# Optimization experiments

Hardware: AMD Instinct MI355X
Metric: run time of the kernel (lower is better)

## Reference

```python
import jax, jax.numpy as jnp
import numpy as np

# ---- config (matches init_kwargs) ----
B, N, D = 16, 300, 256
HEADS, HD = 8, D // 8
FF = 1024
HID = FF // 2                      # SwiGLU hidden
SPATIAL = [(80, 80), (40, 40), (20, 20), (10, 10)]
LVL = len(SPATIAL)
NP = 4                              # points per level
TP = LVL * NP                       # total sampling points = 16
L = sum(h * w for h, w in SPATIAL)  # 8400
EPS = 1e-6


def setup_inputs() -> dict:
    key = jax.random.key(0)
    ks = jax.random.split(key, 24)
    s = 0.02
    return {
        "target": jax.random.normal(ks[0], (B, N, D), jnp.float32),
        "reference_points": jax.random.uniform(ks[1], (B, N, 1, 4), jnp.float32, 0.05, 0.95),
        "memory": jax.random.normal(ks[2], (B, L, D), jnp.float32),
        # self-attention
        "qkv_w": jax.random.normal(ks[3], (3 * D, D), jnp.float32) * s,
        "qkv_b": jnp.zeros((3 * D,), jnp.float32),
        "out_w": jax.random.normal(ks[4], (D, D), jnp.float32) * s,
        "out_b": jnp.zeros((D,), jnp.float32),
        "norm1_w": jnp.ones((D,), jnp.float32),
        # deformable cross-attention
        "off_w": jax.random.normal(ks[5], (HEADS * TP * 2, D), jnp.float32) * s,
        "off_b": jax.random.normal(ks[6], (HEADS * TP * 2,), jnp.float32) * 0.1,
        "aw_w": jax.random.normal(ks[7], (HEADS * TP, D), jnp.float32) * s,
        "aw_b": jnp.zeros((HEADS * TP,), jnp.float32),
        "cout_w": jax.random.normal(ks[8], (D, D), jnp.float32) * s,
        "cout_b": jnp.zeros((D,), jnp.float32),
        "norm2_w": jnp.ones((D,), jnp.float32),
        # SwiGLU FFN
        "w13": jax.random.normal(ks[9], (2 * HID, D), jnp.float32) * s,
        "w13_b": jnp.zeros((2 * HID,), jnp.float32),
        "w2": jax.random.normal(ks[10], (D, HID), jnp.float32) * s,
        "w2_b": jnp.zeros((D,), jnp.float32),
        "norm3_w": jnp.ones((D,), jnp.float32),
    }


def rmsnorm(x, w):
    return x * jax.lax.rsqrt(jnp.mean(x * x, axis=-1, keepdims=True) + EPS) * w


def bilinear_sample(vflat, loc, H, W):
    """vflat: (BH, hd, H*W); loc: (BH, Q, 2) in [0,1]. grid_sample align_corners=False, zero pad."""
    x = loc[..., 0] * W - 0.5
    y = loc[..., 1] * H - 0.5
    x0 = jnp.floor(x); y0 = jnp.floor(y)
    dx = x - x0; dy = y - y0
    x0i = x0.astype(jnp.int32); y0i = y0.astype(jnp.int32)

    def gather(xi, yi, w):
        valid = (xi >= 0) & (xi < W) & (yi >= 0) & (yi < H)
        idx = jnp.clip(yi, 0, H - 1) * W + jnp.clip(xi, 0, W - 1)
        g = jnp.take_along_axis(vflat, idx[:, None, :], axis=2)  # (BH, hd, Q)
        return g * (w * valid)[:, None, :]

    return (gather(x0i, y0i, (1 - dx) * (1 - dy))
            + gather(x0i + 1, y0i, dx * (1 - dy))
            + gather(x0i, y0i + 1, (1 - dx) * dy)
            + gather(x0i + 1, y0i + 1, dx * dy))


def reference(target, reference_points, memory, qkv_w, qkv_b, out_w, out_b, norm1_w,
              off_w, off_b, aw_w, aw_b, cout_w, cout_b, norm2_w,
              w13, w13_b, w2, w2_b, norm3_w):
    # ---------- self-attention (query_pos_embed=None, attn_mask=None) ----------
    qkv = target @ qkv_w.T + qkv_b                    # (B,N,3D)
    qkv = qkv.reshape(B, N, 3, HEADS, HD).transpose(2, 0, 3, 1, 4)
    q, k, v = qkv[0], qkv[1], qkv[2]                  # (B,H,N,hd)
    attn = jax.nn.softmax(jnp.einsum("bhqd,bhkd->bhqk", q, k) / np.sqrt(HD), axis=-1)
    sa = jnp.einsum("bhqk,bhkd->bhqd", attn, v).transpose(0, 2, 1, 3).reshape(B, N, D)
    x = rmsnorm(target + (sa @ out_w.T + out_b), norm1_w)

    # ---------- deformable cross-attention ----------
    # value_op: memory -> per-head value (B,H,hd,L)
    val = memory.reshape(B, L, HEADS, HD).transpose(0, 2, 3, 1).reshape(B * HEADS, HD, L)

    offsets = (x @ off_w.T + off_b).reshape(B, N, HEADS, TP, 2)
    aw = jax.nn.softmax((x @ aw_w.T + aw_b).reshape(B, N, HEADS, TP), axis=-1)

    ref_xy = reference_points[:, :, :, None, :2]      # (B,N,1,1,2)
    ref_wh = reference_points[:, :, :, None, 2:]
    pts_scale = 1.0 / NP
    loc = ref_xy + offsets * pts_scale * ref_wh * 0.5  # (B,N,H,TP,2)
    loc = loc.transpose(0, 2, 1, 3, 4).reshape(B * HEADS, N, TP, 2)

    sampled = []
    start = 0
    for li, (H, W) in enumerate(SPATIAL):
        v_l = jax.lax.dynamic_slice_in_dim(val, start, H * W, axis=2)
        loc_l = loc[:, :, li * NP:(li + 1) * NP, :].reshape(B * HEADS, N * NP, 2)
        s = bilinear_sample(v_l, loc_l, H, W).reshape(B * HEADS, HD, N, NP)
        sampled.append(s)
        start += H * W
    sampled = jnp.concatenate(sampled, axis=-1)        # (BH, hd, N, TP)

    w = aw.transpose(0, 2, 1, 3).reshape(B * HEADS, 1, N, TP)
    ca = (sampled * w).sum(-1)                         # (BH, hd, N)
    ca = ca.reshape(B, HEADS, HD, N).transpose(0, 3, 1, 2).reshape(B, N, D)
    ca = ca @ cout_w.T + cout_b

    x = rmsnorm(x + ca, norm2_w)

    # ---------- SwiGLU FFN ----------
    h = x @ w13.T + w13_b
    h1, h2 = h[..., :HID], h[..., HID:]
    ffn = (jax.nn.silu(h1) * h2) @ w2.T + w2_b
    x = jnp.clip(x + ffn, -65504.0, 65504.0)
    return rmsnorm(x, norm3_w)
```

## Files before the change

kernel.cpp:

```cpp
#include <hip/hip_runtime.h>
#include <cstdint>
#include <cstddef>


typedef __attribute__((ext_vector_type(8))) short bf16x8;
typedef __attribute__((ext_vector_type(4))) float f32x4;

__device__ __forceinline__ unsigned short f2bf(float f) {
  unsigned int u = __float_as_uint(f);
  u = (u + 0x7fffu + ((u >> 16) & 1u)) >> 16;
  return (unsigned short)u;
}
__device__ __forceinline__ unsigned int pack2bf(float lo, float hi) {
  return ((unsigned int)f2bf(hi) << 16) | (unsigned int)f2bf(lo);
}

__device__ __forceinline__ void gemm_dev(
    const float* __restrict__ A, const float* __restrict__ W,
    const float* __restrict__ bias, float* __restrict__ C,
    int N, int K, int row0, int col0,
    unsigned short* As, unsigned short* Ws)
{
  const int t = threadIdx.x, wave = t >> 6, lane = t & 63;
  const int lr = lane & 15, g = lane >> 4;
  const int sr = t >> 4, sc = (t & 15) * 4;

  float4 ra[4], rw[8];
  const float* Ab = A + (size_t)(row0 + sr) * K + sc;
  const float* Wb = W + (size_t)(col0 + sr) * K + sc;

#pragma unroll
  for (int i = 0; i < 4; ++i) ra[i] = *(const float4*)(Ab + (size_t)16 * i * K);
#pragma unroll
  for (int j = 0; j < 8; ++j) rw[j] = *(const float4*)(Wb + (size_t)16 * j * K);

  f32x4 acc[4][2] = {};

  for (int k0 = 0; k0 < K; k0 += 64) {
    __syncthreads();
#pragma unroll
    for (int i = 0; i < 4; ++i) {
      uint2 p;
      p.x = pack2bf(ra[i].x, ra[i].y);
      p.y = pack2bf(ra[i].z, ra[i].w);
      *(uint2*)&As[(sr + 16 * i) * 72 + sc] = p;
    }
#pragma unroll
    for (int j = 0; j < 8; ++j) {
      uint2 p;
      p.x = pack2bf(rw[j].x, rw[j].y);
      p.y = pack2bf(rw[j].z, rw[j].w);
      *(uint2*)&Ws[(sr + 16 * j) * 72 + sc] = p;
    }
    __syncthreads();

    if (k0 + 64 < K) {
#pragma unroll
      for (int i = 0; i < 4; ++i)
        ra[i] = *(const float4*)(Ab + (size_t)16 * i * K + k0 + 64);
#pragma unroll
      for (int j = 0; j < 8; ++j)
        rw[j] = *(const float4*)(Wb + (size_t)16 * j * K + k0 + 64);
    }

#pragma unroll
    for (int ks = 0; ks < 2; ++ks) {
      bf16x8 aA[4], bB[2];
#pragma unroll
      for (int i = 0; i < 4; ++i)
        aA[i] = *(const bf16x8*)&As[(i * 16 + lr) * 72 + ks * 32 + g * 8];
#pragma unroll
      for (int j = 0; j < 2; ++j)
        bB[j] = *(const bf16x8*)&Ws[(wave * 32 + j * 16 + lr) * 72 + ks * 32 + g * 8];
#pragma unroll
      for (int i = 0; i < 4; ++i)
#pragma unroll
        for (int j = 0; j < 2; ++j)
          acc[i][j] = __builtin_amdgcn_mfma_f32_16x16x32_bf16(aA[i], bB[j], acc[i][j], 0, 0, 0);
    }
  }

  const float b0 = bias[col0 + wave * 32 + lr];
  const float b1 = bias[col0 + wave * 32 + 16 + lr];
#pragma unroll
  for (int i = 0; i < 4; ++i) {
#pragma unroll
    for (int r = 0; r < 4; ++r) {
      const int row = row0 + i * 16 + g * 4 + r;
      float* dst = &C[(size_t)row * N + col0 + wave * 32 + lr];
      dst[0]  = acc[i][0][r] + b0;
      dst[16] = acc[i][1][r] + b1;
    }
  }
}

__global__ __launch_bounds__(256) void gemm_mfma(
    const float* __restrict__ A, const float* __restrict__ W,
    const float* __restrict__ bias, float* __restrict__ C, int N, int K)
{
  __shared__ __align__(16) unsigned short As[64 * 72];
  __shared__ __align__(16) unsigned short Ws[128 * 72];
  gemm_dev(A, W, bias, C, N, K, blockIdx.y * 64, blockIdx.x * 128, As, Ws);
}

__global__ __launch_bounds__(256) void gemm_offaw(
    const float* __restrict__ X,
    const float* __restrict__ off_w, const float* __restrict__ off_b, float* __restrict__ OF,
    const float* __restrict__ aw_w, const float* __restrict__ aw_b, float* __restrict__ AW,
    int K)
{
  __shared__ __align__(16) unsigned short As[64 * 72];
  __shared__ __align__(16) unsigned short Ws[128 * 72];
  if (blockIdx.x < 2)
    gemm_dev(X, off_w, off_b, OF, 256, K, blockIdx.y * 64, blockIdx.x * 128, As, Ws);
  else
    gemm_dev(X, aw_w, aw_b, AW, 128, K, blockIdx.y * 64, 0, As, Ws);
}

template <bool SWIGLU>
__global__ __launch_bounds__(256) void gemm_rms32(
    const float* __restrict__ A, const float* __restrict__ W,
    const float* __restrict__ bias, const float* __restrict__ res,
    const float* __restrict__ nw, float* __restrict__ C,
    int K, int clip)
{
  __shared__ __align__(16) unsigned short As[32 * 72];
  __shared__ __align__(16) unsigned short Ws[256 * 72];
  __shared__ float rsum[32][4];

  const int t = threadIdx.x, wave = t >> 6, lane = t & 63;
  const int lr = lane & 15, g = lane >> 4;
  const int row0 = blockIdx.x * 32;
  const int sr = t >> 4, sc = (t & 15) * 4;
  const int Astride = SWIGLU ? 1024 : K;

  float4 ra1[2], ra2[2], rw[16];
  const float* Ab = A + (size_t)(row0 + sr) * Astride + sc;
  const float* Wb = W + (size_t)sr * K + sc;

#pragma unroll
  for (int i = 0; i < 2; ++i) {
    ra1[i] = *(const float4*)(Ab + (size_t)16 * i * Astride);
    if (SWIGLU) ra2[i] = *(const float4*)(Ab + (size_t)16 * i * Astride + 512);
  }
#pragma unroll
  for (int j = 0; j < 16; ++j) rw[j] = *(const float4*)(Wb + (size_t)16 * j * K);

  f32x4 acc[2][4] = {};

  for (int k0 = 0; k0 < K; k0 += 64) {
    __syncthreads();
#pragma unroll
    for (int i = 0; i < 2; ++i) {
      float4 v;
      if (SWIGLU) {
        v.x = ra1[i].x / (1.f + __expf(-ra1[i].x)) * ra2[i].x;
        v.y = ra1[i].y / (1.f + __expf(-ra1[i].y)) * ra2[i].y;
        v.z = ra1[i].z / (1.f + __expf(-ra1[i].z)) * ra2[i].z;
        v.w = ra1[i].w / (1.f + __expf(-ra1[i].w)) * ra2[i].w;
      } else {
        v = ra1[i];
      }
      uint2 p;
      p.x = pack2bf(v.x, v.y);
      p.y = pack2bf(v.z, v.w);
      *(uint2*)&As[(sr + 16 * i) * 72 + sc] = p;
    }
#pragma unroll
    for (int j = 0; j < 16; ++j) {
      uint2 p;
      p.x = pack2bf(rw[j].x, rw[j].y);
      p.y = pack2bf(rw[j].z, rw[j].w);
      *(uint2*)&Ws[(sr + 16 * j) * 72 + sc] = p;
    }
    __syncthreads();

    if (k0 + 64 < K) {
#pragma unroll
      for (int i = 0; i < 2; ++i) {
        ra1[i] = *(const float4*)(Ab + (size_t)16 * i * Astride + k0 + 64);
        if (SWIGLU) ra2[i] = *(const float4*)(Ab + (size_t)16 * i * Astride + 512 + k0 + 64);
      }
#pragma unroll
      for (int j = 0; j < 16; ++j)
        rw[j] = *(const float4*)(Wb + (size_t)16 * j * K + k0 + 64);
    }

#pragma unroll
    for (int ks = 0; ks < 2; ++ks) {
      bf16x8 aA[2], bB[4];
#pragma unroll
      for (int i = 0; i < 2; ++i)
        aA[i] = *(const bf16x8*)&As[(i * 16 + lr) * 72 + ks * 32 + g * 8];
#pragma unroll
      for (int j = 0; j < 4; ++j)
        bB[j] = *(const bf16x8*)&Ws[(wave * 64 + j * 16 + lr) * 72 + ks * 32 + g * 8];
#pragma unroll
      for (int i = 0; i < 2; ++i)
#pragma unroll
        for (int j = 0; j < 4; ++j)
          acc[i][j] = __builtin_amdgcn_mfma_f32_16x16x32_bf16(aA[i], bB[j], acc[i][j], 0, 0, 0);
    }
  }

  float bj[4], wj[4];
#pragma unroll
  for (int j = 0; j < 4; ++j) {
    bj[j] = bias[wave * 64 + j * 16 + lr];
    wj[j] = nw[wave * 64 + j * 16 + lr];
  }

  float part[2][4] = {};
#pragma unroll
  for (int i = 0; i < 2; ++i) {
#pragma unroll
    for (int r = 0; r < 4; ++r) {
      const int row = row0 + i * 16 + g * 4 + r;
#pragma unroll
      for (int j = 0; j < 4; ++j) {
        const int col = wave * 64 + j * 16 + lr;
        float v = acc[i][j][r] + bj[j] + res[(size_t)row * 256 + col];
        if (clip) v = fminf(fmaxf(v, -65504.f), 65504.f);
        acc[i][j][r] = v;
        part[i][r] += v * v;
      }
    }
  }
#pragma unroll
  for (int i = 0; i < 2; ++i)
#pragma unroll
    for (int r = 0; r < 4; ++r) {
      float s = part[i][r];
      s += __shfl_xor(s, 1);
      s += __shfl_xor(s, 2);
      s += __shfl_xor(s, 4);
      s += __shfl_xor(s, 8);
      part[i][r] = s;
    }
  if (lr == 0) {
#pragma unroll
    for (int i = 0; i < 2; ++i)
#pragma unroll
      for (int r = 0; r < 4; ++r)
        rsum[i * 16 + g * 4 + r][wave] = part[i][r];
  }
  __syncthreads();

#pragma unroll
  for (int i = 0; i < 2; ++i) {
#pragma unroll
    for (int r = 0; r < 4; ++r) {
      const int row = row0 + i * 16 + g * 4 + r;
      const f32x4 q = *(const f32x4*)&rsum[i * 16 + g * 4 + r][0];
      const float tot = q[0] + q[1] + q[2] + q[3];
      const float scale = rsqrtf(tot * (1.0f / 256.0f) + 1e-6f);
#pragma unroll
      for (int j = 0; j < 4; ++j) {
        const int col = wave * 64 + j * 16 + lr;
        C[(size_t)row * 256 + col] = acc[i][j][r] * scale * wj[j];
      }
    }
  }
}

__global__ __launch_bounds__(256) void gemm_qkv(
    const float* __restrict__ A, const float* __restrict__ W,
    const float* __restrict__ bias,
    unsigned short* __restrict__ Qb, unsigned short* __restrict__ Kb,
    unsigned short* __restrict__ VTb)
{
  __shared__ __align__(16) unsigned short As[64 * 72];
  __shared__ __align__(16) unsigned short Ws[128 * 72];
  const int K = 256;
  const int t = threadIdx.x, wave = t >> 6, lane = t & 63;
  const int lr = lane & 15, g = lane >> 4;
  const int row0 = blockIdx.y * 64, col0 = blockIdx.x * 128;
  const int sr = t >> 4, sc = (t & 15) * 4;

  float4 ra[4], rw[8];
  const float* Ab = A + (size_t)(row0 + sr) * K + sc;
  const float* Wb = W + (size_t)(col0 + sr) * K + sc;

#pragma unroll
  for (int i = 0; i < 4; ++i) ra[i] = *(const float4*)(Ab + (size_t)16 * i * K);
#pragma unroll
  for (int j = 0; j < 8; ++j) rw[j] = *(const float4*)(Wb + (size_t)16 * j * K);

  f32x4 acc[4][2] = {};

  for (int k0 = 0; k0 < K; k0 += 64) {
    __syncthreads();
#pragma unroll
    for (int i = 0; i < 4; ++i) {
      uint2 p;
      p.x = pack2bf(ra[i].x, ra[i].y);
      p.y = pack2bf(ra[i].z, ra[i].w);
      *(uint2*)&As[(sr + 16 * i) * 72 + sc] = p;
    }
#pragma unroll
    for (int j = 0; j < 8; ++j) {
      uint2 p;
      p.x = pack2bf(rw[j].x, rw[j].y);
      p.y = pack2bf(rw[j].z, rw[j].w);
      *(uint2*)&Ws[(sr + 16 * j) * 72 + sc] = p;
    }
    __syncthreads();

    if (k0 + 64 < K) {
#pragma unroll
      for (int i = 0; i < 4; ++i)
        ra[i] = *(const float4*)(Ab + (size_t)16 * i * K + k0 + 64);
#pragma unroll
      for (int j = 0; j < 8; ++j)
        rw[j] = *(const float4*)(Wb + (size_t)16 * j * K + k0 + 64);
    }

#pragma unroll
    for (int ks = 0; ks < 2; ++ks) {
      bf16x8 aA[4], bB[2];
#pragma unroll
      for (int i = 0; i < 4; ++i)
        aA[i] = *(const bf16x8*)&As[(i * 16 + lr) * 72 + ks * 32 + g * 8];
#pragma unroll
      for (int j = 0; j < 2; ++j)
        bB[j] = *(const bf16x8*)&Ws[(wave * 32 + j * 16 + lr) * 72 + ks * 32 + g * 8];
#pragma unroll
      for (int i = 0; i < 4; ++i)
#pragma unroll
        for (int j = 0; j < 2; ++j)
          acc[i][j] = __builtin_amdgcn_mfma_f32_16x16x32_bf16(aA[i], bB[j], acc[i][j], 0, 0, 0);
    }
  }

  const int bx = blockIdx.x;
  const float scale = 0.17677669529663687f;
  const float b0 = bias[col0 + wave * 32 + lr];
  const float b1 = bias[col0 + wave * 32 + 16 + lr];

  if (bx < 4) {
    unsigned short* dstT = (bx < 2) ? Qb : Kb;
    const float mul = (bx < 2) ? scale : 1.0f;
#pragma unroll
    for (int i = 0; i < 4; ++i) {
#pragma unroll
      for (int r = 0; r < 4; ++r) {
        const int row = row0 + i * 16 + g * 4 + r;
        const int b = row / 300, n = row - b * 300;
#pragma unroll
        for (int j = 0; j < 2; ++j) {
          const int c768 = col0 + wave * 32 + j * 16 + lr;
          const int h = (c768 >> 5) & 7, c = c768 & 31;
          const float v = (acc[i][j][r] + (j ? b1 : b0)) * mul;
          dstT[((size_t)(b * 8 + h) * 304 + n) * 32 + c] = f2bf(v);
        }
      }
    }
  } else {
    __syncthreads();
#pragma unroll
    for (int i = 0; i < 4; ++i)
#pragma unroll
      for (int r = 0; r < 4; ++r)
#pragma unroll
        for (int j = 0; j < 2; ++j) {
          const int c_local = wave * 32 + j * 16 + lr;
          const int n_local = i * 16 + g * 4 + r;
          Ws[c_local * 72 + n_local] = f2bf(acc[i][j][r] + (j ? b1 : b0));
        }
    __syncthreads();
    for (int idx = t; idx < 128 * 64; idx += 256) {
      const int c_local = idx >> 6, n_local = idx & 63;
      const int row = row0 + n_local;
      const int b = row / 300, n = row - b * 300;
      const int c768 = col0 + c_local;
      const int h = (c768 >> 5) & 7, c = c768 & 31;
      VTb[((size_t)(b * 8 + h) * 32 + c) * 320 + n] = Ws[c_local * 72 + n_local];
    }
    if (blockIdx.y == 74) {
      for (int idx = t; idx < 64 * 32 * 20; idx += 256) {
        const int n = 300 + idx % 20;
        const int rem = idx / 20;
        const int c = rem & 31, bh4 = rem >> 5;
        const int b = bh4 >> 2, h = (bx - 4) * 4 + (bh4 & 3);
        VTb[((size_t)(b * 8 + h) * 32 + c) * 320 + n] = 0;
      }
    }
  }
}

__global__ __launch_bounds__(64) void attn_core(
    const unsigned short* __restrict__ Qb, const unsigned short* __restrict__ Kb,
    const unsigned short* __restrict__ VTb, float* __restrict__ sa)
{
  __shared__ __align__(16) unsigned short P[16 * 40];
  const int gt = blockIdx.x;
  const int bh = blockIdx.y, b = bh >> 3, h = bh & 7;
  const int lane = threadIdx.x, lr = lane & 15, g = lane >> 4;

  const unsigned short* Kbase = Kb + (size_t)bh * 304 * 32;
  const unsigned short* Vbase = VTb + (size_t)bh * 32 * 320;

  bf16x8 aQ = *(const bf16x8*)&Qb[((size_t)bh * 304 + gt * 16 + lr) * 32 + g * 8];

  f32x4 s[19];
  const f32x4 zero = {0.f, 0.f, 0.f, 0.f};
#pragma unroll
  for (int kt = 0; kt < 19; ++kt) {
    bf16x8 bK = *(const bf16x8*)&Kbase[(kt * 16 + lr) * 32 + g * 8];
    s[kt] = __builtin_amdgcn_mfma_f32_16x16x32_bf16(aQ, bK, zero, 0, 0, 0);
  }
  if (lr >= 12) {
    s[18][0] = -1e30f; s[18][1] = -1e30f; s[18][2] = -1e30f; s[18][3] = -1e30f;
  }

  float inv[4];
#pragma unroll
  for (int r = 0; r < 4; ++r) {
    float m = -1e30f;
#pragma unroll
    for (int kt = 0; kt < 19; ++kt) m = fmaxf(m, s[kt][r]);
#pragma unroll
    for (int o = 8; o >= 1; o >>= 1) m = fmaxf(m, __shfl_xor(m, o));
    float sum = 0.f;
#pragma unroll
    for (int kt = 0; kt < 19; ++kt) {
      float e = __expf(s[kt][r] - m);
      s[kt][r] = e;
      sum += e;
    }
#pragma unroll
    for (int o = 8; o >= 1; o >>= 1) sum += __shfl_xor(sum, o);
    inv[r] = 1.f / sum;
  }

  f32x4 o0 = {0.f, 0.f, 0.f, 0.f}, o1 = {0.f, 0.f, 0.f, 0.f};
#pragma unroll
  for (int ks = 0; ks < 10; ++ks) {
#pragma unroll
    for (int tp = 0; tp < 2; ++tp) {
      const int kt = ks * 2 + tp;
#pragma unroll
      for (int r = 0; r < 4; ++r) {
        unsigned short pv = (kt < 19) ? f2bf(s[kt][r]) : (unsigned short)0;
        P[(g * 4 + r) * 40 + tp * 16 + lr] = pv;
      }
    }
    asm volatile("s_waitcnt lgkmcnt(0)" ::: "memory");
    __builtin_amdgcn_sched_barrier(0);
    bf16x8 aP = *(const bf16x8*)&P[lr * 40 + g * 8];
    bf16x8 bV0 = *(const bf16x8*)&Vbase[(size_t)lr * 320 + ks * 32 + g * 8];
    bf16x8 bV1 = *(const bf16x8*)&Vbase[(size_t)(16 + lr) * 320 + ks * 32 + g * 8];
    o0 = __builtin_amdgcn_mfma_f32_16x16x32_bf16(aP, bV0, o0, 0, 0, 0);
    o1 = __builtin_amdgcn_mfma_f32_16x16x32_bf16(aP, bV1, o1, 0, 0, 0);
  }

#pragma unroll
  for (int r = 0; r < 4; ++r) {
    const int q = gt * 16 + g * 4 + r;
    if (q < 300) {
      const float iv = inv[r];
      float* dst = &sa[((size_t)b * 300 + q) * 256 + h * 32];
      dst[lr] = o0[r] * iv;
      dst[16 + lr] = o1[r] * iv;
    }
  }
}

__global__ __launch_bounds__(256) void deform_k(
    const float* __restrict__ memory, const float* __restrict__ refp,
    const float* __restrict__ OFF, const float* __restrict__ AW,
    float* __restrict__ ca)
{
  __shared__ float locx[8][16], locy[8][16], wgt[8][16];
  const int bn = blockIdx.x, b = bn / 300, t = threadIdx.x;

  if (t < 128) {
    int h = t >> 4, p = t & 15;
    float cx = refp[(size_t)bn * 4 + 0], cy = refp[(size_t)bn * 4 + 1];
    float rw = refp[(size_t)bn * 4 + 2], rh = refp[(size_t)bn * 4 + 3];
    float ox = OFF[(size_t)bn * 256 + h * 32 + p * 2 + 0];
    float oy = OFF[(size_t)bn * 256 + h * 32 + p * 2 + 1];
    locx[h][p] = cx + ox * 0.125f * rw;
    locy[h][p] = cy + oy * 0.125f * rh;
    float av = AW[(size_t)bn * 128 + t];
    float mx = av;
#pragma unroll
    for (int o = 8; o; o >>= 1) mx = fmaxf(mx, __shfl_xor(mx, o));
    float e = __expf(av - mx);
    float ssum = e;
#pragma unroll
    for (int o = 8; o; o >>= 1) ssum += __shfl_xor(ssum, o);
    wgt[h][p] = e / ssum;
  }
  __syncthreads();

  const int h = t >> 5, hd = t & 31;
  const float* mb = memory + (size_t)b * 8500 * 256 + h * 32 + hd;
  float acc = 0.f;
#pragma unroll
  for (int p = 0; p < 16; ++p) {
    const int HWs[4] = {80, 40, 20, 10};
    const int Sts[4] = {0, 6400, 8000, 8400};
    const int li = p >> 2;
    const int Hh = HWs[li], Ww = HWs[li], st = Sts[li];
    float x = locx[h][p] * (float)Ww - 0.5f;
    float y = locy[h][p] * (float)Hh - 0.5f;
    float x0f = floorf(x), y0f = floorf(y);
    float dx = x - x0f, dy = y - y0f;
    int x0 = (int)x0f, y0 = (int)y0f;
    float awp = wgt[h][p];
#pragma unroll
    for (int cc = 0; cc < 4; ++cc) {
      int xi = x0 + (cc & 1), yi = y0 + (cc >> 1);
      float wc = ((cc & 1) ? dx : 1.f - dx) * ((cc >> 1) ? dy : 1.f - dy);
      bool valid = (xi >= 0) && (xi < Ww) && (yi >= 0) && (yi < Hh);
      int xc = xi < 0 ? 0 : (xi >= Ww ? Ww - 1 : xi);
      int yc = yi < 0 ? 0 : (yi >= Hh ? Hh - 1 : yi);
      float gv = mb[(size_t)(st + yc * Ww + xc) * 256];
      acc += gv * (valid ? wc * awp : 0.f);
    }
  }
  ca[(size_t)bn * 256 + t] = acc;
}

extern "C" void kernel_launch(void* const* d_in, const int* in_sizes, int n_in,
                              void* d_out, int out_size, void* d_ws, size_t ws_size,
                              hipStream_t stream)
{
  (void)in_sizes; (void)n_in; (void)out_size; (void)ws_size;
  const float* target  = (const float*)d_in[0];
  const float* refp    = (const float*)d_in[1];
  const float* memory  = (const float*)d_in[2];
  const float* qkv_w   = (const float*)d_in[3];
  const float* qkv_b   = (const float*)d_in[4];
  const float* out_w   = (const float*)d_in[5];
  const float* out_b   = (const float*)d_in[6];
  const float* norm1_w = (const float*)d_in[7];
  const float* off_w   = (const float*)d_in[8];
  const float* off_b   = (const float*)d_in[9];
  const float* aw_w    = (const float*)d_in[10];
  const float* aw_b    = (const float*)d_in[11];
  const float* cout_w  = (const float*)d_in[12];
  const float* cout_b  = (const float*)d_in[13];
  const float* norm2_w = (const float*)d_in[14];
  const float* w13     = (const float*)d_in[15];
  const float* w13_b   = (const float*)d_in[16];
  const float* w2      = (const float*)d_in[17];
  const float* w2_b    = (const float*)d_in[18];
  const float* norm3_w = (const float*)d_in[19];
  float* out = (float*)d_out;

  float* ws  = (float*)d_ws;
  float* SA  = ws;
  float* X   = SA  + 4800 * 256;
  float* OF  = X   + 4800 * 256;
  float* AWb = OF  + 4800 * 256;
  float* CA  = AWb + 4800 * 128;
  float* X2  = CA  + 4800 * 256;
  float* Hb  = X2  + 4800 * 256;
  unsigned short* Qb  = (unsigned short*)(Hb + 4800 * 1024);
  unsigned short* Kb  = Qb + 128 * 304 * 32;
  unsigned short* VTb = Kb + 128 * 304 * 32;

  dim3 blk(256);

  gemm_qkv<<<dim3(6, 75), blk, 0, stream>>>(target, qkv_w, qkv_b, Qb, Kb, VTb);
  attn_core<<<dim3(19, 128), dim3(64), 0, stream>>>(Qb, Kb, VTb, SA);
  gemm_rms32<false><<<150, blk, 0, stream>>>(SA, out_w, out_b, target, norm1_w, X, 256, 0);
  gemm_offaw<<<dim3(3, 75), blk, 0, stream>>>(X, off_w, off_b, OF, aw_w, aw_b, AWb, 256);
  deform_k<<<4800, blk, 0, stream>>>(memory, refp, OF, AWb, CA);
  gemm_rms32<false><<<150, blk, 0, stream>>>(CA, cout_w, cout_b, X, norm2_w, X2, 256, 0);
  gemm_mfma<<<dim3(8, 75), blk, 0, stream>>>(X2, w13, w13_b, Hb, 1024, 256);
  gemm_rms32<true><<<150, blk, 0, stream>>>(Hb, w2, w2_b, X2, norm3_w, out, 512, 1);
}
```

Measured before the change: 131.0 us.

## Pre-convert weights and activations to bf16 so GEMMs load bf16 directly

Adds a conversion kernel that turns the target and all weight matrices into bf16 at the start of every call. Intermediate activations (self-attention output, deformable output, normed X and X2) are also written as bf16 mirrors. The GEMMs then load bf16 tiles with 16-byte loads and skip per-tile packing. This halves global read traffic and removes conversion ALU work inside the GEMM loops, at the cost of one extra launch and extra bf16 writes.

```diff
diff --git a/kernel.cpp b/kernel.cpp
--- a/kernel.cpp
+++ b/kernel.cpp
@@ -15,52 +15,83 @@
   return ((unsigned int)f2bf(hi) << 16) | (unsigned int)f2bf(lo);
 }
 
-__device__ __forceinline__ void gemm_dev(
-    const float* __restrict__ A, const float* __restrict__ W,
-    const float* __restrict__ bias, float* __restrict__ C,
-    int N, int K, int row0, int col0,
-    unsigned short* As, unsigned short* Ws)
+__global__ __launch_bounds__(256) void conv_w(
+    const float* __restrict__ s0, const float* __restrict__ s1,
+    const float* __restrict__ s2, const float* __restrict__ s3,
+    const float* __restrict__ s4, const float* __restrict__ s5,
+    const float* __restrict__ s6, const float* __restrict__ s7,
+    unsigned short* __restrict__ d0, unsigned short* __restrict__ d1,
+    unsigned short* __restrict__ d2, unsigned short* __restrict__ d3,
+    unsigned short* __restrict__ d4, unsigned short* __restrict__ d5,
+    unsigned short* __restrict__ d6, unsigned short* __restrict__ d7)
+{
+  const int sizes[8] = {1228800, 196608, 65536, 65536, 32768, 65536, 262144, 131072};
+  const float* s; unsigned short* d;
+  switch (blockIdx.y) {
+    case 0: s = s0; d = d0; break;
+    case 1: s = s1; d = d1; break;
+    case 2: s = s2; d = d2; break;
+    case 3: s = s3; d = d3; break;
+    case 4: s = s4; d = d4; break;
+    case 5: s = s5; d = d5; break;
+    case 6: s = s6; d = d6; break;
+    default: s = s7; d = d7; break;
+  }
+  const int n = sizes[blockIdx.y];
+  const int i4 = (blockIdx.x * 256 + threadIdx.x) * 4;
+  if (i4 >= n) return;
+  float4 v = *(const float4*)&s[i4];
+  uint2 p;
+  p.x = pack2bf(v.x, v.y);
+  p.y = pack2bf(v.z, v.w);
+  *(uint2*)&d[i4] = p;
+}
+
+__device__ __forceinline__ void gemm_core16(
+    const unsigned short* __restrict__ A16, const unsigned short* __restrict__ W16,
+    int K, int row0, int col0,
+    unsigned short* As, unsigned short* Ws, f32x4 acc[4][2])
 {
   const int t = threadIdx.x, wave = t >> 6, lane = t & 63;
   const int lr = lane & 15, g = lane >> 4;
-  const int sr = t >> 4, sc = (t & 15) * 4;
-
-  float4 ra[4], rw[8];
-  const float* Ab = A + (size_t)(row0 + sr) * K + sc;
-  const float* Wb = W + (size_t)(col0 + sr) * K + sc;
-
-#pragma unroll
-  for (int i = 0; i < 4; ++i) ra[i] = *(const float4*)(Ab + (size_t)16 * i * K);
-#pragma unroll
-  for (int j = 0; j < 8; ++j) rw[j] = *(const float4*)(Wb + (size_t)16 * j * K);
-
-  f32x4 acc[4][2] = {};
+
+  uint4 rA[2], rW[4];
+#pragma unroll
+  for (int i = 0; i < 2; ++i) {
+    const int c = t + i * 256, row = c >> 3, sl = c & 7;
+    rA[i] = *(const uint4*)&A16[(size_t)(row0 + row) * K + sl * 8];
+  }
+#pragma unroll
+  for (int j = 0; j < 4; ++j) {
+    const int c = t + j * 256, row = c >> 3, sl = c & 7;
+    rW[j] = *(const uint4*)&W16[(size_t)(col0 + row) * K + sl * 8];
+  }
 
   for (int k0 = 0; k0 < K; k0 += 64) {
     __syncthreads();
 #pragma unroll
-    for (int i = 0; i < 4; ++i) {
-      uint2 p;
-      p.x = pack2bf(ra[i].x, ra[i].y);
-      p.y = pack2bf(ra[i].z, ra[i].w);
-      *(uint2*)&As[(sr + 16 * i) * 72 + sc] = p;
-    }
-#pragma unroll
-    for (int j = 0; j < 8; ++j) {
-      uint2 p;
-      p.x = pack2bf(rw[j].x, rw[j].y);
-      p.y = pack2bf(rw[j].z, rw[j].w);
-      *(uint2*)&Ws[(sr + 16 * j) * 72 + sc] = p;
+    for (int i = 0; i < 2; ++i) {
+      const int c = t + i * 256, row = c >> 3, sl = c & 7;
+      *(uint4*)&As[row * 72 + sl * 8] = rA[i];
+    }
+#pragma unroll
+    for (int j = 0; j < 4; ++j) {
+      const int c = t + j * 256, row = c >> 3, sl = c & 7;
+      *(uint4*)&Ws[row * 72 + sl * 8] = rW[j];
     }
     __syncthreads();
 
     if (k0 + 64 < K) {
 #pragma unroll
-      for (int i = 0; i < 4; ++i)
-        ra[i] = *(const float4*)(Ab + (size_t)16 * i * K + k0 + 64);
-#pragma unroll
-      for (int j = 0; j < 8; ++j)
-        rw[j] = *(const float4*)(Wb + (size_t)16 * j * K + k0 + 64);
+      for (int i = 0; i < 2; ++i) {
+        const int c = t + i * 256, row = c >> 3, sl = c & 7;
+        rA[i] = *(const uint4*)&A16[(size_t)(row0 + row) * K + k0 + 64 + sl * 8];
+      }
+#pragma unroll
+      for (int j = 0; j < 4; ++j) {
+        const int c = t + j * 256, row = c >> 3, sl = c & 7;
+        rW[j] = *(const uint4*)&W16[(size_t)(col0 + row) * K + k0 + 64 + sl * 8];
+      }
     }
 
 #pragma unroll
@@ -79,7 +110,20 @@
           acc[i][j] = __builtin_amdgcn_mfma_f32_16x16x32_bf16(aA[i], bB[j], acc[i][j], 0, 0, 0);
     }
   }
-
+}
+
+__global__ __launch_bounds__(256) void gemm_mfma16(
+    const unsigned short* __restrict__ A16, const unsigned short* __restrict__ W16,
+    const float* __restrict__ bias, float* __restrict__ C, int N, int K)
+{
+  __shared__ __align__(16) unsigned short As[64 * 72];
+  __shared__ __align__(16) unsigned short Ws[128 * 72];
+  const int row0 = blockIdx.y * 64, col0 = blockIdx.x * 128;
+  f32x4 acc[4][2] = {};
+  gemm_core16(A16, W16, K, row0, col0, As, Ws, acc);
+
+  const int t = threadIdx.x, wave = t >> 6, lane = t & 63;
+  const int lr = lane & 15, g = lane >> 4;
   const float b0 = bias[col0 + wave * 32 + lr];
   const float b1 = bias[col0 + wave * 32 + 16 + lr];
 #pragma unroll
@@ -94,244 +138,56 @@
   }
 }
 
-__global__ __launch_bounds__(256) void gemm_mfma(
-    const float* __restrict__ A, const float* __restrict__ W,
-    const float* __restrict__ bias, float* __restrict__ C, int N, int K)
+__global__ __launch_bounds__(256) void gemm_offaw16(
+    const unsigned short* __restrict__ X16,
+    const unsigned short* __restrict__ off16, const float* __restrict__ off_b,
+    float* __restrict__ OF,
+    const unsigned short* __restrict__ aw16, const float* __restrict__ aw_b,
+    float* __restrict__ AW)
 {
   __shared__ __align__(16) unsigned short As[64 * 72];
   __shared__ __align__(16) unsigned short Ws[128 * 72];
-  gemm_dev(A, W, bias, C, N, K, blockIdx.y * 64, blockIdx.x * 128, As, Ws);
-}
-
-__global__ __launch_bounds__(256) void gemm_offaw(
-    const float* __restrict__ X,
-    const float* __restrict__ off_w, const float* __restrict__ off_b, float* __restrict__ OF,
-    const float* __restrict__ aw_w, const float* __restrict__ aw_b, float* __restrict__ AW,
-    int K)
-{
-  __shared__ __align__(16) unsigned short As[64 * 72];
-  __shared__ __align__(16) unsigned short Ws[128 * 72];
-  if (blockIdx.x < 2)
-    gemm_dev(X, off_w, off_b, OF, 256, K, blockIdx.y * 64, blockIdx.x * 128, As, Ws);
-  else
-    gemm_dev(X, aw_w, aw_b, AW, 128, K, blockIdx.y * 64, 0, As, Ws);
-}
-
-template <bool SWIGLU>
-__global__ __launch_bounds__(256) void gemm_rms32(
-    const float* __restrict__ A, const float* __restrict__ W,
-    const float* __restrict__ bias, const float* __restrict__ res,
-    const float* __restrict__ nw, float* __restrict__ C,
-    int K, int clip)
-{
-  __shared__ __align__(16) unsigned short As[32 * 72];
-  __shared__ __align__(16) unsigned short Ws[256 * 72];
-  __shared__ float rsum[32][4];
+  const int row0 = blockIdx.y * 64;
+  const bool isOff = blockIdx.x < 2;
+  const int col0 = isOff ? blockIdx.x * 128 : 0;
+  const unsigned short* W16 = isOff ? off16 : aw16;
+  const float* bias = isOff ? off_b : aw_b;
+  float* C = isOff ? OF : AW;
+  const int N = isOff ? 256 : 128;
+
+  f32x4 acc[4][2] = {};
+  gemm_core16(X16, W16, 256, row0, col0, As, Ws, acc);
 
   const int t = threadIdx.x, wave = t >> 6, lane = t & 63;
   const int lr = lane & 15, g = lane >> 4;
-  const int row0 = blockIdx.x * 32;
-  const int sr = t >> 4, sc = (t & 15) * 4;
-  const int Astride = SWIGLU ? 1024 : K;
-
-  float4 ra1[2], ra2[2], rw[16];
-  const float* Ab = A + (size_t)(row0 + sr) * Astride + sc;
-  const float* Wb = W + (size_t)sr * K + sc;
-
-#pragma unroll
-  for (int i = 0; i < 2; ++i) {
-    ra1[i] = *(const float4*)(Ab + (size_t)16 * i * Astride);
-    if (SWIGLU) ra2[i] = *(const float4*)(Ab + (size_t)16 * i * Astride + 512);
-  }
-#pragma unroll
-  for (int j = 0; j < 16; ++j) rw[j] = *(const float4*)(Wb + (size_t)16 * j * K);
-
-  f32x4 acc[2][4] = {};
-
-  for (int k0 = 0; k0 < K; k0 += 64) {
-    __syncthreads();
-#pragma unroll
-    for (int i = 0; i < 2; ++i) {
-      float4 v;
-      if (SWIGLU) {
-        v.x = ra1[i].x / (1.f + __expf(-ra1[i].x)) * ra2[i].x;
-        v.y = ra1[i].y / (1.f + __expf(-ra1[i].y)) * ra2[i].y;
-        v.z = ra1[i].z / (1.f + __expf(-ra1[i].z)) * ra2[i].z;
-        v.w = ra1[i].w / (1.f + __expf(-ra1[i].w)) * ra2[i].w;
-      } else {
-        v = ra1[i];
-      }
-      uint2 p;
-      p.x = pack2bf(v.x, v.y);
-      p.y = pack2bf(v.z, v.w);
-      *(uint2*)&As[(sr + 16 * i) * 72 + sc] = p;
-    }
-#pragma unroll
-    for (int j = 0; j < 16; ++j) {
-      uint2 p;
-      p.x = pack2bf(rw[j].x, rw[j].y);
-      p.y = pack2bf(rw[j].z, rw[j].w);
-      *(uint2*)&Ws[(sr + 16 * j) * 72 + sc] = p;
-    }
-    __syncthreads();
-
-    if (k0 + 64 < K) {
-#pragma unroll
-      for (int i = 0; i < 2; ++i) {
-        ra1[i] = *(const float4*)(Ab + (size_t)16 * i * Astride + k0 + 64);
-        if (SWIGLU) ra2[i] = *(const float4*)(Ab + (size_t)16 * i * Astride + 512 + k0 + 64);
-      }
-#pragma unroll
-      for (int j = 0; j < 16; ++j)
-        rw[j] = *(const float4*)(Wb + (size_t)16 * j * K + k0 + 64);
-    }
-
-#pragma unroll
-    for (int ks = 0; ks < 2; ++ks) {
-      bf16x8 aA[2], bB[4];
-#pragma unroll
-      for (int i = 0; i < 2; ++i)
-        aA[i] = *(const bf16x8*)&As[(i * 16 + lr) * 72 + ks * 32 + g * 8];
-#pragma unroll
-      for (int j = 0; j < 4; ++j)
-        bB[j] = *(const bf16x8*)&Ws[(wave * 64 + j * 16 + lr) * 72 + ks * 32 + g * 8];
-#pragma unroll
-      for (int i = 0; i < 2; ++i)
-#pragma unroll
-        for (int j = 0; j < 4; ++j)
-          acc[i][j] = __builtin_amdgcn_mfma_f32_16x16x32_bf16(aA[i], bB[j], acc[i][j], 0, 0, 0);
-    }
-  }
-
-  float bj[4], wj[4];
-#pragma unroll
-  for (int j = 0; j < 4; ++j) {
-    bj[j] = bias[wave * 64 + j * 16 + lr];
-    wj[j] = nw[wave * 64 + j * 16 + lr];
-  }
-
-  float part[2][4] = {};
-#pragma unroll
-  for (int i = 0; i < 2; ++i) {
+  const float b0 = bias[col0 + wave * 32 + lr];
+  const float b1 = bias[col0 + wave * 32 + 16 + lr];
+#pragma unroll
+  for (int i = 0; i < 4; ++i) {
 #pragma unroll
     for (int r = 0; r < 4; ++r) {
       const int row = row0 + i * 16 + g * 4 + r;
-#pragma unroll
-      for (int j = 0; j < 4; ++j) {
-        const int col = wave * 64 + j * 16 + lr;
-        float v = acc[i][j][r] + bj[j] + res[(size_t)row * 256 + col];
-        if (clip) v = fminf(fmaxf(v, -65504.f), 65504.f);
-        acc[i][j][r] = v;
-        part[i][r] += v * v;
-      }
-    }
-  }
-#pragma unroll
-  for (int i = 0; i < 2; ++i)
-#pragma unroll
-    for (int r = 0; r < 4; ++r) {
-      float s = part[i][r];
-      s += __shfl_xor(s, 1);
-      s += __shfl_xor(s, 2);
-      s += __shfl_xor(s, 4);
-      s += __shfl_xor(s, 8);
-      part[i][r] = s;
-    }
-  if (lr == 0) {
-#pragma unroll
-    for (int i = 0; i < 2; ++i)
-#pragma unroll
-      for (int r = 0; r < 4; ++r)
-        rsum[i * 16 + g * 4 + r][wave] = part[i][r];
-  }
-  __syncthreads();
-
-#pragma unroll
-  for (int i = 0; i < 2; ++i) {
-#pragma unroll
-    for (int r = 0; r < 4; ++r) {
-      const int row = row0 + i * 16 + g * 4 + r;
-      const f32x4 q = *(const f32x4*)&rsum[i * 16 + g * 4 + r][0];
-      const float tot = q[0] + q[1] + q[2] + q[3];
-      const float scale = rsqrtf(tot * (1.0f / 256.0f) + 1e-6f);
-#pragma unroll
-      for (int j = 0; j < 4; ++j) {
-        const int col = wave * 64 + j * 16 + lr;
-        C[(size_t)row * 256 + col] = acc[i][j][r] * scale * wj[j];
-      }
-    }
-  }
-}
-
-__global__ __launch_bounds__(256) void gemm_qkv(
-    const float* __restrict__ A, const float* __restrict__ W,
+      float* dst = &C[(size_t)row * N + col0 + wave * 32 + lr];
+      dst[0]  = acc[i][0][r] + b0;
+      dst[16] = acc[i][1][r] + b1;
+    }
+  }
+}
+
+__global__ __launch_bounds__(256) void gemm_qkv16(
+    const unsigned short* __restrict__ T16, const unsigned short* __restrict__ W16,
     const float* __restrict__ bias,
     unsigned short* __restrict__ Qb, unsigned short* __restrict__ Kb,
     unsigned short* __restrict__ VTb)
 {
   __shared__ __align__(16) unsigned short As[64 * 72];
   __shared__ __align__(16) unsigned short Ws[128 * 72];
-  const int K = 256;
+  const int row0 = blockIdx.y * 64, col0 = blockIdx.x * 128;
+  f32x4 acc[4][2] = {};
+  gemm_core16(T16, W16, 256, row0, col0, As, Ws, acc);
+
   const int t = threadIdx.x, wave = t >> 6, lane = t & 63;
   const int lr = lane & 15, g = lane >> 4;
-  const int row0 = blockIdx.y * 64, col0 = blockIdx.x * 128;
-  const int sr = t >> 4, sc = (t & 15) * 4;
-
-  float4 ra[4], rw[8];
-  const float* Ab = A + (size_t)(row0 + sr) * K + sc;
-  const float* Wb = W + (size_t)(col0 + sr) * K + sc;
-
-#pragma unroll
-  for (int i = 0; i < 4; ++i) ra[i] = *(const float4*)(Ab + (size_t)16 * i * K);
-#pragma unroll
-  for (int j = 0; j < 8; ++j) rw[j] = *(const float4*)(Wb + (size_t)16 * j * K);
-
-  f32x4 acc[4][2] = {};
-
-  for (int k0 = 0; k0 < K; k0 += 64) {
-    __syncthreads();
-#pragma unroll
-    for (int i = 0; i < 4; ++i) {
-      uint2 p;
-      p.x = pack2bf(ra[i].x, ra[i].y);
-      p.y = pack2bf(ra[i].z, ra[i].w);
-      *(uint2*)&As[(sr + 16 * i) * 72 + sc] = p;
-    }
-#pragma unroll
-    for (int j = 0; j < 8; ++j) {
-      uint2 p;
-      p.x = pack2bf(rw[j].x, rw[j].y);
-      p.y = pack2bf(rw[j].z, rw[j].w);
-      *(uint2*)&Ws[(sr + 16 * j) * 72 + sc] = p;
-    }
-    __syncthreads();
-
-    if (k0 + 64 < K) {
-#pragma unroll
-      for (int i = 0; i < 4; ++i)
-        ra[i] = *(const float4*)(Ab + (size_t)16 * i * K + k0 + 64);
-#pragma unroll
-      for (int j = 0; j < 8; ++j)
-        rw[j] = *(const float4*)(Wb + (size_t)16 * j * K + k0 + 64);
-    }
-
-#pragma unroll
-    for (int ks = 0; ks < 2; ++ks) {
-      bf16x8 aA[4], bB[2];
-#pragma unroll
-      for (int i = 0; i < 4; ++i)
-        aA[i] = *(const bf16x8*)&As[(i * 16 + lr) * 72 + ks * 32 + g * 8];
-#pragma unroll
-      for (int j = 0; j < 2; ++j)
-        bB[j] = *(const bf16x8*)&Ws[(wave * 32 + j * 16 + lr) * 72 + ks * 32 + g * 8];
-#pragma unroll
-      for (int i = 0; i < 4; ++i)
-#pragma unroll
-        for (int j = 0; j < 2; ++j)
-          acc[i][j] = __builtin_amdgcn_mfma_f32_16x16x32_bf16(aA[i], bB[j], acc[i][j], 0, 0, 0);
-    }
-  }
-
   const int bx = blockIdx.x;
   const float scale = 0.17677669529663687f;
   const float b0 = bias[col0 + wave * 32 + lr];
@@ -388,9 +244,172 @@
   }
 }
 
+template <bool SWIGLU>
+__global__ __launch_bounds__(256) void gemm_rms32_16(
+    const void* __restrict__ Ain, const unsigned short* __restrict__ W16,
+    const float* __restrict__ bias, const float* __restrict__ res,
+    const float* __restrict__ nw, float* __restrict__ C,
+    unsigned short* __restrict__ Cmir, int K, int clip)
+{
+  __shared__ __align__(16) unsigned short As[32 * 72];
+  __shared__ __align__(16) unsigned short Ws[256 * 72];
+  __shared__ float rsum[32][4];
+
+  const int t = threadIdx.x, wave = t >> 6, lane = t & 63;
+  const int lr = lane & 15, g = lane >> 4;
+  const int row0 = blockIdx.x * 32;
+  const int sr = t >> 4, sc = (t & 15) * 4;
+
+  uint4 rA;
+  float4 ra1[2], ra2[2];
+  uint4 rW[8];
+  const unsigned short* A16 = (const unsigned short*)Ain;
+  const float* Af = (const float*)Ain;
+
+  if (SWIGLU) {
+#pragma unroll
+    for (int i = 0; i < 2; ++i) {
+      ra1[i] = *(const float4*)&Af[(size_t)(row0 + sr + 16 * i) * 1024 + sc];
+      ra2[i] = *(const float4*)&Af[(size_t)(row0 + sr + 16 * i) * 1024 + 512 + sc];
+    }
+  } else {
+    const int row = t >> 3, sl = t & 7;
+    rA = *(const uint4*)&A16[(size_t)(row0 + row) * K + sl * 8];
+  }
+#pragma unroll
+  for (int j = 0; j < 8; ++j) {
+    const int c = t + j * 256, row = c >> 3, sl = c & 7;
+    rW[j] = *(const uint4*)&W16[(size_t)row * K + sl * 8];
+  }
+
+  f32x4 acc[2][4] = {};
+
+  for (int k0 = 0; k0 < K; k0 += 64) {
+    __syncthreads();
+    if (SWIGLU) {
+#pragma unroll
+      for (int i = 0; i < 2; ++i) {
+        float4 v;
+        v.x = ra1[i].x / (1.f + __expf(-ra1[i].x)) * ra2[i].x;
+        v.y = ra1[i].y / (1.f + __expf(-ra1[i].y)) * ra2[i].y;
+        v.z = ra1[i].z / (1.f + __expf(-ra1[i].z)) * ra2[i].z;
+        v.w = ra1[i].w / (1.f + __expf(-ra1[i].w)) * ra2[i].w;
+        uint2 p;
+        p.x = pack2bf(v.x, v.y);
+        p.y = pack2bf(v.z, v.w);
+        *(uint2*)&As[(sr + 16 * i) * 72 + sc] = p;
+      }
+    } else {
+      const int row = t >> 3, sl = t & 7;
+      *(uint4*)&As[row * 72 + sl * 8] = rA;
+    }
+#pragma unroll
+    for (int j = 0; j < 8; ++j) {
+      const int c = t + j * 256, row = c >> 3, sl = c & 7;
+      *(uint4*)&Ws[row * 72 + sl * 8] = rW[j];
+    }
+    __syncthreads();
+
+    if (k0 + 64 < K) {
+      if (SWIGLU) {
+#pragma unroll
+        for (int i = 0; i < 2; ++i) {
+          ra1[i] = *(const float4*)&Af[(size_t)(row0 + sr + 16 * i) * 1024 + k0 + 64 + sc];
+          ra2[i] = *(const float4*)&Af[(size_t)(row0 + sr + 16 * i) * 1024 + 512 + k0 + 64 + sc];
+        }
+      } else {
+        const int row = t >> 3, sl = t & 7;
+        rA = *(const uint4*)&A16[(size_t)(row0 + row) * K + k0 + 64 + sl * 8];
+      }
+#pragma unroll
+      for (int j = 0; j < 8; ++j) {
+        const int c = t + j * 256, row = c >> 3, sl = c & 7;
+        rW[j] = *(const uint4*)&W16[(size_t)row * K + k0 + 64 + sl * 8];
+      }
+    }
+
+#pragma unroll
+    for (int ks = 0; ks < 2; ++ks) {
+      bf16x8 aA[2], bB[4];
+#pragma unroll
+      for (int i = 0; i < 2; ++i)
+        aA[i] = *(const bf16x8*)&As[(i * 16 + lr) * 72 + ks * 32 + g * 8];
+#pragma unroll
+      for (int j = 0; j < 4; ++j)
+        bB[j] = *(const bf16x8*)&Ws[(wave * 64 + j * 16 + lr) * 72 + ks * 32 + g * 8];
+#pragma unroll
+      for (int i = 0; i < 2; ++i)
+#pragma unroll
+        for (int j = 0; j < 4; ++j)
+          acc[i][j] = __builtin_amdgcn_mfma_f32_16x16x32_bf16(aA[i], bB[j], acc[i][j], 0, 0, 0);
+    }
+  }
+
+  float bj[4], wj[4];
+#pragma unroll
+  for (int j = 0; j < 4; ++j) {
+    bj[j] = bias[wave * 64 + j * 16 + lr];
+    wj[j] = nw[wave * 64 + j * 16 + lr];
+  }
+
+  float part[2][4] = {};
+#pragma unroll
+  for (int i = 0; i < 2; ++i) {
+#pragma unroll
+    for (int r = 0; r < 4; ++r) {
+      const int row = row0 + i * 16 + g * 4 + r;
+#pragma unroll
+      for (int j = 0; j < 4; ++j) {
+        const int col = wave * 64 + j * 16 + lr;
+        float v = acc[i][j][r] + bj[j] + res[(size_t)row * 256 + col];
+        if (clip) v = fminf(fmaxf(v, -65504.f), 65504.f);
+        acc[i][j][r] = v;
+        part[i][r] += v * v;
+      }
+    }
+  }
+#pragma unroll
+  for (int i = 0; i < 2; ++i)
+#pragma unroll
+    for (int r = 0; r < 4; ++r) {
+      float s = part[i][r];
+      s += __shfl_xor(s, 1);
+      s += __shfl_xor(s, 2);
+      s += __shfl_xor(s, 4);
+      s += __shfl_xor(s, 8);
+      part[i][r] = s;
+    }
+  if (lr == 0) {
+#pragma unroll
+    for (int i = 0; i < 2; ++i)
+#pragma unroll
+      for (int r = 0; r < 4; ++r)
+        rsum[i * 16 + g * 4 + r][wave] = part[i][r];
+  }
+  __syncthreads();
+
+#pragma unroll
+  for (int i = 0; i < 2; ++i) {
+#pragma unroll
+    for (int r = 0; r < 4; ++r) {
+      const int row = row0 + i * 16 + g * 4 + r;
+      const f32x4 q = *(const f32x4*)&rsum[i * 16 + g * 4 + r][0];
+      const float tot = q[0] + q[1] + q[2] + q[3];
+      const float scale = rsqrtf(tot * (1.0f / 256.0f) + 1e-6f);
+#pragma unroll
+      for (int j = 0; j < 4; ++j) {
+        const int col = wave * 64 + j * 16 + lr;
+        const float o = acc[i][j][r] * scale * wj[j];
+        C[(size_t)row * 256 + col] = o;
+        if (Cmir) Cmir[(size_t)row * 256 + col] = f2bf(o);
+      }
+    }
+  }
+}
+
 __global__ __launch_bounds__(64) void attn_core(
     const unsigned short* __restrict__ Qb, const unsigned short* __restrict__ Kb,
-    const unsigned short* __restrict__ VTb, float* __restrict__ sa)
+    const unsigned short* __restrict__ VTb, unsigned short* __restrict__ sa16)
 {
   __shared__ __align__(16) unsigned short P[16 * 40];
   const int gt = blockIdx.x;
@@ -459,9 +478,9 @@
     const int q = gt * 16 + g * 4 + r;
     if (q < 300) {
       const float iv = inv[r];
-      float* dst = &sa[((size_t)b * 300 + q) * 256 + h * 32];
-      dst[lr] = o0[r] * iv;
-      dst[16 + lr] = o1[r] * iv;
+      unsigned short* dst = &sa16[((size_t)b * 300 + q) * 256 + h * 32];
+      dst[lr] = f2bf(o0[r] * iv);
+      dst[16 + lr] = f2bf(o1[r] * iv);
     }
   }
 }
@@ -469,7 +488,7 @@
 __global__ __launch_bounds__(256) void deform_k(
     const float* __restrict__ memory, const float* __restrict__ refp,
     const float* __restrict__ OFF, const float* __restrict__ AW,
-    float* __restrict__ ca)
+    unsigned short* __restrict__ ca16)
 {
   __shared__ float locx[8][16], locy[8][16], wgt[8][16];
   const int bn = blockIdx.x, b = bn / 300, t = threadIdx.x;
@@ -520,7 +539,7 @@
       acc += gv * (valid ? wc * awp : 0.f);
     }
   }
-  ca[(size_t)bn * 256 + t] = acc;
+  ca16[(size_t)bn * 256 + t] = f2bf(acc);
 }
 
 extern "C" void kernel_launch(void* const* d_in, const int* in_sizes, int n_in,
@@ -551,25 +570,40 @@
   float* out = (float*)d_out;
 
   float* ws  = (float*)d_ws;
-  float* SA  = ws;
-  float* X   = SA  + 4800 * 256;
+  float* X   = ws;
   float* OF  = X   + 4800 * 256;
   float* AWb = OF  + 4800 * 256;
-  float* CA  = AWb + 4800 * 128;
-  float* X2  = CA  + 4800 * 256;
+  float* X2  = AWb + 4800 * 128;
   float* Hb  = X2  + 4800 * 256;
-  unsigned short* Qb  = (unsigned short*)(Hb + 4800 * 1024);
-  unsigned short* Kb  = Qb + 128 * 304 * 32;
-  unsigned short* VTb = Kb + 128 * 304 * 32;
+
+  unsigned short* u   = (unsigned short*)(Hb + 4800 * 1024);
+  unsigned short* Qb  = u;
+  unsigned short* Kb  = Qb  + 1245184;
+  unsigned short* VTb = Kb  + 1245184;
+  unsigned short* SA16 = VTb + 1310720;
+  unsigned short* CA16 = SA16 + 1228800;
+  unsigned short* X16  = CA16 + 1228800;
+  unsigned short* X216 = X16  + 1228800;
+  unsigned short* T16  = X216 + 1228800;
+  unsigned short* qkv16  = T16  + 1228800;
+  unsigned short* out16  = qkv16  + 196608;
+  unsigned short* off16  = out16  + 65536;
+  unsigned short* aw16   = off16  + 65536;
+  unsigned short* cout16 = aw16   + 32768;
+  unsigned short* w13_16 = cout16 + 65536;
+  unsigned short* w2_16  = w13_16 + 262144;
 
   dim3 blk(256);
 
-  gemm_qkv<<<dim3(6, 75), blk, 0, stream>>>(target, qkv_w, qkv_b, Qb, Kb, VTb);
-  attn_core<<<dim3(19, 128), dim3(64), 0, stream>>>(Qb, Kb, VTb, SA);
-  gemm_rms32<false><<<150, blk, 0, stream>>>(SA, out_w, out_b, target, norm1_w, X, 256, 0);
-  gemm_offaw<<<dim3(3, 75), blk, 0, stream>>>(X, off_w, off_b, OF, aw_w, aw_b, AWb, 256);
-  deform_k<<<4800, blk, 0, stream>>>(memory, refp, OF, AWb, CA);
-  gemm_rms32<false><<<150, blk, 0, stream>>>(CA, cout_w, cout_b, X, norm2_w, X2, 256, 0);
-  gemm_mfma<<<dim3(8, 75), blk, 0, stream>>>(X2, w13, w13_b, Hb, 1024, 256);
-  gemm_rms32<true><<<150, blk, 0, stream>>>(Hb, w2, w2_b, X2, norm3_w, out, 512, 1);
-}
+  conv_w<<<dim3(1200, 8), blk, 0, stream>>>(
+      target, qkv_w, out_w, off_w, aw_w, cout_w, w13, w2,
+      T16, qkv16, out16, off16, aw16, cout16, w13_16, w2_16);
+  gemm_qkv16<<<dim3(6, 75), blk, 0, stream>>>(T16, qkv16, qkv_b, Qb, Kb, VTb);
+  attn_core<<<dim3(19, 128), dim3(64), 0, stream>>>(Qb, Kb, VTb, SA16);
+  gemm_rms32_16<false><<<150, blk, 0, stream>>>(SA16, out16, out_b, target, norm1_w, X, X16, 256, 0);
+  gemm_offaw16<<<dim3(3, 75), blk, 0, stream>>>(X16, off16, off_b, OF, aw16, aw_b, AWb);
+  deform_k<<<4800, blk, 0, stream>>>(memory, refp, OF, AWb, CA16);
+  gemm_rms32_16<false><<<150, blk, 0, stream>>>(CA16, cout16, cout_b, X, norm2_w, X2, X216, 256, 0);
+  gemm_mfma16<<<dim3(8, 75), blk, 0, stream>>>(X216, w13_16, w13_b, Hb, 1024, 256);
+  gemm_rms32_16<true><<<150, blk, 0, stream>>>(Hb, w2_16, w2_b, X2, norm3_w, out, nullptr, 512, 1);
+}
```

Result: slower. 177.0 us (+35.1%).
